# Optimization experiments

Hardware: AMD Instinct MI355X
Metric: run time of the kernel (lower is better)

Reference implementation:

```python
import jax, jax.numpy as jnp
import numpy as np

# ---- model / data constants ----
B, N, D, L = 32, 96, 64, 5          # graphs, nodes per graph, hidden, layers
EP = 768                             # directed edges per graph (symmetrized in to_dense)
NODE_VOCAB = 11                      # matches LocalFWL2(..., 11, 5, 'instance')
EDGE_VOCAB = 5                       # edge labels 0..4; index 5 = 'no edge' embedding row
EPS = 1e-5


def setup_inputs() -> dict:
    key = jax.random.key(0)
    ks = jax.random.split(key, 12)
    # block-contiguous batch: graph b owns nodes [b*N, (b+1)*N)
    x = jax.random.randint(ks[0], (B * N,), 0, NODE_VOCAB)
    u = jax.random.randint(ks[1], (B, EP), 0, N)
    v = jax.random.randint(ks[2], (B, EP), 0, N)
    off = (jnp.arange(B) * N)[:, None]
    edge_index = jnp.stack([(u + off).reshape(-1), (v + off).reshape(-1)], axis=0)
    edge_attr = jax.random.randint(ks[3], (B * EP,), 0, EDGE_VOCAB)
    s = 0.1
    inv = 1.0 / np.sqrt(D)
    return {
        "x": x,
        "edge_index": edge_index,
        "edge_attr": edge_attr,
        "node_emb": jax.random.normal(ks[4], (NODE_VOCAB, D), jnp.float32) * s,
        "edge_emb": jax.random.normal(ks[5], (EDGE_VOCAB + 1, D), jnp.float32) * s,
        "W1": jax.random.normal(ks[6], (L, D, D), jnp.float32) * inv,
        "b1": jnp.zeros((L, D), jnp.float32),
        "W2": jax.random.normal(ks[7], (L, D, D), jnp.float32) * inv,
        "b2": jnp.zeros((L, D), jnp.float32),
        "Wm": jax.random.normal(ks[8], (L, D, D), jnp.float32) * inv,
        "bm": jnp.zeros((L, D), jnp.float32),
        "gamma": jnp.ones((L, D), jnp.float32),
        "beta": jnp.zeros((L, D), jnp.float32),
        "pool_w": jax.random.normal(ks[9], (D, 1), jnp.float32) * inv,
        "pool_b": jnp.zeros((1,), jnp.float32),
    }


def reference(x, edge_index, edge_attr, node_emb, edge_emb,
              W1, b1, W2, b2, Wm, bm, gamma, beta, pool_w, pool_b):
    # ---- to_dense: sparse edge list -> dense per-graph edge-label matrix ----
    g = edge_index[0] // N
    u = edge_index[0] % N
    v = edge_index[1] % N
    A = jnp.full((B, N, N), EDGE_VOCAB, dtype=jnp.int32)        # EDGE_VOCAB = no-edge
    ea = edge_attr.astype(jnp.int32)
    A = A.at[g, u, v].set(ea)
    A = A.at[g, v, u].set(ea)                                    # undirected
    adj = (A != EDGE_VOCAB).astype(node_emb.dtype)               # [B,N,N]

    # ---- pair-state init: W_uv = h_u + h_v + edge_emb(A_uv) ----
    H = node_emb[x.reshape(B, N)]                                # [B,N,D]
    W = H[:, :, None, :] + H[:, None, :, :] + edge_emb[A]        # [B,N,N,D]

    # ---- local FWL(2) layers ----
    for l in range(L):
        h1 = jax.nn.relu(jnp.einsum('buwd,de->buwe', W, W1[l]) + b1[l])
        h2 = jax.nn.relu(jnp.einsum('bwvd,de->bwve', W, W2[l]) + b2[l])
        # aggregate over w restricted to neighbors of v (local FWL2)
        M = jnp.einsum('buwd,bwv,bwvd->buvd', h1, adj, h2)       # [B,N,N,D]
        W = W + jnp.einsum('buvd,de->buve', M, Wm[l]) + bm[l]
        # instance norm over the pair dims (u,v), per graph, per channel
        mu = W.mean(axis=(1, 2), keepdims=True)
        var = W.var(axis=(1, 2), keepdims=True)
        W = gamma[l] * (W - mu) * jax.lax.rsqrt(var + EPS) + beta[l]
        W = jax.nn.relu(W)

    # ---- pooling: sum over all pairs, then Linear(D, 1), squeeze ----
    pooled = W.sum(axis=(1, 2))                                  # [B,D]
    return (pooled @ pool_w + pool_b).squeeze(-1)                # [B]
```

## Files before the change

### kernel.cpp

```cpp
#include <hip/hip_runtime.h>
#include <hip/hip_bf16.h>

#define B_ 32
#define N_ 96
#define D_ 64
#define L_ 5
#define BE_ 24576
#define NN_ 9216
#define BNN_ 294912
#define EPS_ 1e-5f
#define INV_NN (1.0f/9216.0f)

typedef unsigned short u16;
typedef unsigned int u32;
typedef __attribute__((ext_vector_type(8))) short bf16x8;
typedef __attribute__((ext_vector_type(4))) float f32x4;

__device__ __forceinline__ float bf2f(u16 r){ return __uint_as_float(((u32)r) << 16); }
__device__ __forceinline__ u32 f2bf(float f){
  u32 u = __float_as_uint(f);
  return (u + 0x7fffu + ((u >> 16) & 1u)) >> 16;
}
__device__ __forceinline__ u32 pack2(float lo, float hi){
  return f2bf(lo) | (f2bf(hi) << 16);
}

__global__ void k_scatter(const int* __restrict__ ei, const int* __restrict__ ea,
                          int* __restrict__ A)
{
  int e = blockIdx.x * 256 + threadIdx.x;
  if (e >= BE_) return;
  int a = ei[e], bnode = ei[BE_ + e];
  int g = a / N_;
  int u = a % N_;
  int v = bnode % N_;
  int lab = ea[e] & 7;
  int base = g * NN_;
  atomicMax(&A[base + u * N_ + v], ((e + 1) << 3) | lab);
  atomicMax(&A[base + v * N_ + u], ((BE_ + e + 1) << 3) | lab);
}

__launch_bounds__(256)
__global__ void k_winit(const int* __restrict__ x, const int* __restrict__ A,
                        const float* __restrict__ nemb, const float* __restrict__ eemb,
                        u16* __restrict__ W)
{
  int gid = blockIdx.x * 256 + threadIdx.x;
  int d = (gid & 31) * 2;
  int p = gid >> 5;
  int b = p / NN_;
  int rem = p % NN_;
  int u = rem / N_;
  int v = rem % N_;
  int xu = x[b * N_ + u], xv = x[b * N_ + v];
  int pk = A[p];
  int lab = pk ? (pk & 7) : 5;
  float v0 = nemb[xu * 64 + d]     + nemb[xv * 64 + d]     + eemb[lab * 64 + d];
  float v1 = nemb[xu * 64 + d + 1] + nemb[xv * 64 + d + 1] + eemb[lab * 64 + d + 1];
  ((u32*)W)[gid] = pack2(v0, v1);
}

__global__ void k_prep(const float* __restrict__ W1, const float* __restrict__ W2,
                       const float* __restrict__ Wm, u16* __restrict__ WT)
{
  int idx = blockIdx.x * 256 + threadIdx.x;
  if (idx >= 15 * 4096) return;
  int l3 = idx >> 12;
  int r  = idx & 4095;
  int e = r >> 6, d = r & 63;
  int l = l3 / 3, which = l3 % 3;
  const float* s = which == 0 ? W1 : which == 1 ? W2 : Wm;
  WT[idx] = (u16)f2bf(s[l * 4096 + d * 64 + e]);
}

__global__ void k_ns(const float* __restrict__ st, const float* __restrict__ gm,
                     const float* __restrict__ bt, float* __restrict__ ns)
{
  int i = blockIdx.x * 256 + threadIdx.x;
  if (i >= B_ * 64) return;
  int d = i & 63;
  float S1 = st[i * 2], S2 = st[i * 2 + 1];
  float mu = S1 * INV_NN;
  float var = fmaf(S2, INV_NN, -mu * mu);
  float rsig = rsqrtf(var + EPS_);
  float sc = gm[d] * rsig;
  ns[i * 2] = sc;
  ns[i * 2 + 1] = fmaf(-mu, sc, bt[d]);
}

__launch_bounds__(256)
__global__ void k_lin2(const u16* __restrict__ W, const u16* __restrict__ WT1,
                       const u16* __restrict__ WT2,
                       const float* __restrict__ b1l, const float* __restrict__ b2l,
                       const int* __restrict__ A, const float* __restrict__ ns,
                       int use_norm, u16* __restrict__ h1, u16* __restrict__ g2)
{
  __shared__ u16 Cs[64 * 264];
  const int tid = threadIdx.x;
  const int wave = tid >> 6, lane = tid & 63;
  const int lm = lane & 15, lg = lane >> 4;
  const int b = blockIdx.x / 36;
  const int qbase = (blockIdx.x % 36) * 256;

  float sc[2][8], sh[2][8];
  if (use_norm) {
    #pragma unroll
    for (int s = 0; s < 2; ++s)
      #pragma unroll
      for (int jj = 0; jj < 8; jj += 2) {
        float4 t = *(const float4*)(ns + ((size_t)b * 64 + s * 32 + lg * 8 + jj) * 2);
        sc[s][jj] = t.x; sh[s][jj] = t.y; sc[s][jj + 1] = t.z; sh[s][jj + 1] = t.w;
      }
  } else {
    #pragma unroll
    for (int s = 0; s < 2; ++s)
      #pragma unroll
      for (int j = 0; j < 8; ++j) { sc[s][j] = 1.f; sh[s][j] = 0.f; }
  }

  bf16x8 bF[4][2];
  int flags[4];
  #pragma unroll
  for (int qt = 0; qt < 4; ++qt) {
    int q = qbase + wave * 64 + qt * 16 + lm;
    const u16* wrow = W + ((size_t)b * NN_ + q) * 64;
    flags[qt] = A[b * NN_ + q];
    #pragma unroll
    for (int s = 0; s < 2; ++s) {
      bf16x8 raw = *(const bf16x8*)(wrow + s * 32 + lg * 8);
      if (use_norm) {
        bf16x8 bb;
        #pragma unroll
        for (int j = 0; j < 8; ++j) {
          float v = bf2f((u16)raw[j]);
          v = fmaxf(fmaf(v, sc[s][j], sh[s][j]), 0.f);
          bb[j] = (short)f2bf(v);
        }
        bF[qt][s] = bb;
      } else {
        bF[qt][s] = raw;
      }
    }
  }

  const f32x4 zf = {0.f, 0.f, 0.f, 0.f};

  {
    bf16x8 aF[4][2];
    #pragma unroll
    for (int et = 0; et < 4; ++et)
      #pragma unroll
      for (int s = 0; s < 2; ++s)
        aF[et][s] = *(const bf16x8*)(WT1 + (et * 16 + lm) * 64 + s * 32 + lg * 8);
    f32x4 acc[4][4];
    #pragma unroll
    for (int i = 0; i < 4; ++i)
      #pragma unroll
      for (int j = 0; j < 4; ++j) acc[i][j] = zf;
    #pragma unroll
    for (int qt = 0; qt < 4; ++qt)
      #pragma unroll
      for (int s = 0; s < 2; ++s)
        #pragma unroll
        for (int et = 0; et < 4; ++et)
          acc[qt][et] = __builtin_amdgcn_mfma_f32_16x16x32_bf16(aF[et][s], bF[qt][s], acc[qt][et], 0, 0, 0);
    #pragma unroll
    for (int et = 0; et < 4; ++et) {
      float4 bs = *(const float4*)(b1l + et * 16 + lg * 4);
      float bv[4] = {bs.x, bs.y, bs.z, bs.w};
      #pragma unroll
      for (int qt = 0; qt < 4; ++qt) {
        int col = wave * 64 + qt * 16 + lm;
        #pragma unroll
        for (int r = 0; r < 4; ++r)
          Cs[(et * 16 + lg * 4 + r) * 264 + col] = (u16)f2bf(fmaxf(acc[qt][et][r] + bv[r], 0.f));
      }
    }
  }
  __syncthreads();
  {
    u16* ob = h1 + (size_t)b * 64 * NN_ + qbase;
    for (int i = tid; i < 2048; i += 256) {
      int e = i >> 5, qc = (i & 31) * 8;
      uint4 val = *(const uint4*)&Cs[e * 264 + qc];
      *(uint4*)(ob + (size_t)e * NN_ + qc) = val;
    }
  }
  __syncthreads();

  {
    bf16x8 aF[4][2];
    #pragma unroll
    for (int et = 0; et < 4; ++et)
      #pragma unroll
      for (int s = 0; s < 2; ++s)
        aF[et][s] = *(const bf16x8*)(WT2 + (et * 16 + lm) * 64 + s * 32 + lg * 8);
    f32x4 acc[4][4];
    #pragma unroll
    for (int i = 0; i < 4; ++i)
      #pragma unroll
      for (int j = 0; j < 4; ++j) acc[i][j] = zf;
    #pragma unroll
    for (int qt = 0; qt < 4; ++qt)
      #pragma unroll
      for (int s = 0; s < 2; ++s)
        #pragma unroll
        for (int et = 0; et < 4; ++et)
          acc[qt][et] = __builtin_amdgcn_mfma_f32_16x16x32_bf16(aF[et][s], bF[qt][s], acc[qt][et], 0, 0, 0);
    #pragma unroll
    for (int et = 0; et < 4; ++et) {
      float4 bs = *(const float4*)(b2l + et * 16 + lg * 4);
      float bv[4] = {bs.x, bs.y, bs.z, bs.w};
      #pragma unroll
      for (int qt = 0; qt < 4; ++qt) {
        int col = wave * 64 + qt * 16 + lm;
        #pragma unroll
        for (int r = 0; r < 4; ++r) {
          float v = fmaxf(acc[qt][et][r] + bv[r], 0.f);
          if (!flags[qt]) v = 0.f;
          Cs[(et * 16 + lg * 4 + r) * 264 + col] = (u16)f2bf(v);
        }
      }
    }
  }
  __syncthreads();
  {
    u16* ob = g2 + (size_t)b * 64 * NN_ + qbase;
    for (int i = tid; i < 2048; i += 256) {
      int e = i >> 5, qc = (i & 31) * 8;
      uint4 val = *(const uint4*)&Cs[e * 264 + qc];
      *(uint4*)(ob + (size_t)e * NN_ + qc) = val;
    }
  }
}

__launch_bounds__(256)
__global__ void k_einsum(const u16* __restrict__ h1, const u16* __restrict__ g2n,
                         u16* __restrict__ M)
{
  __shared__ u32 Bt[96 * 60];
  u16* Cst = (u16*)Bt;
  const int tid = threadIdx.x;
  const int wave = tid >> 6, lane = tid & 63;
  const int lm = lane & 15, lg = lane >> 4;
  const int bd = blockIdx.x;
  const u16* h1p = h1 + (size_t)bd * NN_;
  const u16* g2p = g2n + (size_t)bd * NN_;
  const int u0 = (wave & 1) * 48, v0 = (wave >> 1) * 48;

  #pragma unroll
  for (int it = 0; it < 9; ++it) {
    int p = it * 256 + tid;
    int wp = p / 48, vh = (p % 48) * 2;
    u32 a = *(const u32*)(g2p + (2 * wp) * 96 + vh);
    u32 c = *(const u32*)(g2p + (2 * wp + 1) * 96 + vh);
    Bt[vh * 60 + wp]       = (a & 0xffffu) | (c << 16);
    Bt[(vh + 1) * 60 + wp] = (a >> 16) | (c & 0xffff0000u);
  }
  __syncthreads();

  bf16x8 aF[3][3];
  #pragma unroll
  for (int t = 0; t < 3; ++t)
    #pragma unroll
    for (int s = 0; s < 3; ++s)
      aF[t][s] = *(const bf16x8*)(h1p + (u0 + t * 16 + lm) * 96 + s * 32 + lg * 8);

  bf16x8 bF[3][3];
  #pragma unroll
  for (int vt = 0; vt < 3; ++vt)
    #pragma unroll
    for (int s = 0; s < 3; ++s)
      bF[vt][s] = *(const bf16x8*)&Bt[(v0 + vt * 16 + lm) * 60 + s * 16 + lg * 4];
  __syncthreads();

  const f32x4 zf = {0.f, 0.f, 0.f, 0.f};
  f32x4 acc[3][3];
  #pragma unroll
  for (int i = 0; i < 3; ++i)
    #pragma unroll
    for (int j = 0; j < 3; ++j) acc[i][j] = zf;
  #pragma unroll
  for (int s = 0; s < 3; ++s)
    #pragma unroll
    for (int ut = 0; ut < 3; ++ut)
      #pragma unroll
      for (int vt = 0; vt < 3; ++vt)
        acc[ut][vt] = __builtin_amdgcn_mfma_f32_16x16x32_bf16(aF[ut][s], bF[vt][s], acc[ut][vt], 0, 0, 0);

  #pragma unroll
  for (int ut = 0; ut < 3; ++ut)
    #pragma unroll
    for (int vt = 0; vt < 3; ++vt)
      #pragma unroll
      for (int r = 0; r < 4; ++r)
        Cst[(u0 + ut * 16 + lg * 4 + r) * 104 + v0 + vt * 16 + lm] = (u16)f2bf(acc[ut][vt][r]);
  __syncthreads();
  u16* Mp = M + (size_t)bd * NN_;
  for (int i = tid; i < 1152; i += 256) {
    int u = i / 12, vc = (i % 12) * 8;
    uint4 val = *(const uint4*)&Cst[u * 104 + vc];
    *(uint4*)(Mp + u * 96 + vc) = val;
  }
}

__launch_bounds__(256)
__global__ void k_update(const u16* __restrict__ M, const u16* __restrict__ WmT,
                         const float* __restrict__ bml, u16* __restrict__ W,
                         const float* __restrict__ ns, int use_norm,
                         float* __restrict__ sto)
{
  __shared__ u16 Mt[128 * 64];
  __shared__ float red[128];
  const int tid = threadIdx.x;
  const int wave = tid >> 6, lane = tid & 63;
  const int lm = lane & 15, lg = lane >> 4;
  const int b = blockIdx.x / 72;
  const int qblk = (blockIdx.x % 72) * 128;

  if (tid < 128) red[tid] = 0.f;

  {
    const int ql = (tid & 63) + ((tid >> 6) & 1) * 64;
    const int d0 = (tid >> 7) * 32;
    const size_t gbase = (size_t)(b * 64) * NN_ + qblk + ql;
    #pragma unroll
    for (int dd = 0; dd < 32; ++dd) {
      int d = d0 + dd;
      u16 m = M[gbase + (size_t)d * NN_];
      int swz = (d >> 3) ^ (ql & 7);
      Mt[ql * 64 + swz * 8 + (d & 7)] = m;
    }
  }
  __syncthreads();

  bf16x8 aF[4][2];
  #pragma unroll
  for (int et = 0; et < 4; ++et)
    #pragma unroll
    for (int s = 0; s < 2; ++s)
      aF[et][s] = *(const bf16x8*)(WmT + (et * 16 + lm) * 64 + s * 32 + lg * 8);

  const f32x4 zf = {0.f, 0.f, 0.f, 0.f};
  f32x4 acc[2][4];
  #pragma unroll
  for (int i = 0; i < 2; ++i)
    #pragma unroll
    for (int j = 0; j < 4; ++j) acc[i][j] = zf;

  #pragma unroll
  for (int qtL = 0; qtL < 2; ++qtL) {
    int ql = (wave * 2 + qtL) * 16 + lm;
    bf16x8 bF[2];
    #pragma unroll
    for (int s = 0; s < 2; ++s) {
      int slot = s * 4 + lg;
      bF[s] = *(const bf16x8*)&Mt[ql * 64 + ((slot ^ (ql & 7)) * 8)];
    }
    #pragma unroll
    for (int s = 0; s < 2; ++s)
      #pragma unroll
      for (int et = 0; et < 4; ++et)
        acc[qtL][et] = __builtin_amdgcn_mfma_f32_16x16x32_bf16(aF[et][s], bF[s], acc[qtL][et], 0, 0, 0);
  }

  float s1[4][4], s2[4][4];
  #pragma unroll
  for (int i = 0; i < 4; ++i)
    #pragma unroll
    for (int j = 0; j < 4; ++j) { s1[i][j] = 0.f; s2[i][j] = 0.f; }

  #pragma unroll
  for (int et = 0; et < 4; ++et) {
    float4 bs = *(const float4*)(bml + et * 16 + lg * 4);
    float bv[4] = {bs.x, bs.y, bs.z, bs.w};
    float scn[4], shn[4];
    if (use_norm) {
      float4 t0 = *(const float4*)(ns + ((size_t)b * 64 + et * 16 + lg * 4) * 2);
      float4 t1 = *(const float4*)(ns + ((size_t)b * 64 + et * 16 + lg * 4) * 2 + 4);
      scn[0] = t0.x; shn[0] = t0.y; scn[1] = t0.z; shn[1] = t0.w;
      scn[2] = t1.x; shn[2] = t1.y; scn[3] = t1.z; shn[3] = t1.w;
    } else {
      #pragma unroll
      for (int r = 0; r < 4; ++r) { scn[r] = 1.f; shn[r] = 0.f; }
    }
    #pragma unroll
    for (int qtL = 0; qtL < 2; ++qtL) {
      int qg = qblk + (wave * 2 + qtL) * 16 + lm;
      u16* Wp = W + ((size_t)b * NN_ + qg) * 64 + et * 16 + lg * 4;
      uint2 wo = *(const uint2*)Wp;
      float wv[4] = {bf2f((u16)(wo.x & 0xffff)), bf2f((u16)(wo.x >> 16)),
                     bf2f((u16)(wo.y & 0xffff)), bf2f((u16)(wo.y >> 16))};
      float o[4];
      #pragma unroll
      for (int r = 0; r < 4; ++r) {
        float res = use_norm ? fmaxf(fmaf(wv[r], scn[r], shn[r]), 0.f) : wv[r];
        float val = acc[qtL][et][r] + bv[r] + res;
        o[r] = val;
        s1[et][r] += val;
        s2[et][r] = fmaf(val, val, s2[et][r]);
      }
      uint2 ov;
      ov.x = pack2(o[0], o[1]);
      ov.y = pack2(o[2], o[3]);
      *(uint2*)Wp = ov;
    }
  }

  #pragma unroll
  for (int et = 0; et < 4; ++et)
    #pragma unroll
    for (int r = 0; r < 4; ++r) {
      float a = s1[et][r], c = s2[et][r];
      a += __shfl_xor(a, 1, 64); a += __shfl_xor(a, 2, 64);
      a += __shfl_xor(a, 4, 64); a += __shfl_xor(a, 8, 64);
      c += __shfl_xor(c, 1, 64); c += __shfl_xor(c, 2, 64);
      c += __shfl_xor(c, 4, 64); c += __shfl_xor(c, 8, 64);
      if (lm == 0) {
        int e = et * 16 + lg * 4 + r;
        atomicAdd(&red[e], a);
        atomicAdd(&red[64 + e], c);
      }
    }
  __syncthreads();
  if (tid < 64) atomicAdd(&sto[((size_t)b * 64 + tid) * 2], red[tid]);
  else if (tid < 128) atomicAdd(&sto[((size_t)b * 64 + (tid - 64)) * 2 + 1], red[tid]);
}

__launch_bounds__(256)
__global__ void k_pool(const u16* __restrict__ W,
                       const float* __restrict__ st,
                       const float* __restrict__ gml, const float* __restrict__ btl,
                       const float* __restrict__ pw, const float* __restrict__ pb,
                       float* __restrict__ out)
{
  const int b = blockIdx.x / 24;
  const int chunk = blockIdx.x % 24;
  const int tid = threadIdx.x;
  const int e = tid & 63;
  float S1 = st[(b * 64 + e) * 2], S2 = st[(b * 64 + e) * 2 + 1];
  float mu = S1 * INV_NN;
  float var = fmaf(S2, INV_NN, -mu * mu);
  float rsig = rsqrtf(var + EPS_);
  float scl = gml[e] * rsig;
  float shf = fmaf(-mu, scl, btl[e]);
  float pwv = pw[e];
  const u16* base = W + (size_t)b * NN_ * 64 + chunk * 24576;
  float s = 0.f;
  for (int k = 0; k < 96; k++) {
    float w = bf2f(base[k * 256 + tid]);
    s += fmaxf(fmaf(w, scl, shf), 0.f) * pwv;
  }
  for (int o = 32; o; o >>= 1) s += __shfl_down(s, o, 64);
  __shared__ float rs[4];
  if ((tid & 63) == 0) rs[tid >> 6] = s;
  __syncthreads();
  if (tid == 0) {
    float t = rs[0] + rs[1] + rs[2] + rs[3];
    if (chunk == 0) t += pb[0];
    atomicAdd(&out[b], t);
  }
}

extern "C" void kernel_launch(void* const* d_in, const int* in_sizes, int n_in,
                              void* d_out, int out_size, void* d_ws, size_t ws_size,
                              hipStream_t stream) {
  const int*   x    = (const int*)d_in[0];
  const int*   ei   = (const int*)d_in[1];
  const int*   ea   = (const int*)d_in[2];
  const float* nemb = (const float*)d_in[3];
  const float* eemb = (const float*)d_in[4];
  const float* W1   = (const float*)d_in[5];
  const float* b1   = (const float*)d_in[6];
  const float* W2   = (const float*)d_in[7];
  const float* b2   = (const float*)d_in[8];
  const float* Wm   = (const float*)d_in[9];
  const float* bm   = (const float*)d_in[10];
  const float* gm   = (const float*)d_in[11];
  const float* bt   = (const float*)d_in[12];
  const float* pw   = (const float*)d_in[13];
  const float* pb   = (const float*)d_in[14];

  char* ws = (char*)d_ws;
  const size_t OFF_A  = 0;
  const size_t OFF_W  = 1179648;
  const size_t OFF_H1 = 38928384;
  const size_t OFF_G2 = 76677120;
  const size_t OFF_M  = 114425856;
  const size_t OFF_ST = 152174592;
  const size_t OFF_NS = 152190976;
  const size_t OFF_WT = 152207360;
  const size_t NEED   = OFF_WT + 122880;
  if (ws_size < NEED) return;

  int*   A     = (int*)(ws + OFF_A);
  u16*   W     = (u16*)(ws + OFF_W);
  u16*   h1    = (u16*)(ws + OFF_H1);
  u16*   g2n   = (u16*)(ws + OFF_G2);
  u16*   M     = (u16*)(ws + OFF_M);
  float* stats = (float*)(ws + OFF_ST);
  float* ns    = (float*)(ws + OFF_NS);
  u16*   WT    = (u16*)(ws + OFF_WT);
  float* out   = (float*)d_out;

  hipMemsetAsync(A, 0, 1179648, stream);
  hipMemsetAsync(stats, 0, 16384, stream);
  hipMemsetAsync(out, 0, 32 * sizeof(float), stream);

  k_prep<<<240, 256, 0, stream>>>(W1, W2, Wm, WT);
  k_scatter<<<96, 256, 0, stream>>>(ei, ea, A);
  k_winit<<<36864, 256, 0, stream>>>(x, A, nemb, eemb, W);

  for (int l = 0; l < L_; l++) {
    int un = (l > 0);
    if (un) {
      k_ns<<<8, 256, 0, stream>>>(stats, gm + (l - 1) * 64, bt + (l - 1) * 64, ns);
      hipMemsetAsync(stats, 0, 16384, stream);
    }
    k_lin2<<<1152, 256, 0, stream>>>(W, WT + (l * 3 + 0) * 4096, WT + (l * 3 + 1) * 4096,
                                     b1 + l * 64, b2 + l * 64, A, ns, un, h1, g2n);
    k_einsum<<<2048, 256, 0, stream>>>(h1, g2n, M);
    k_update<<<2304, 256, 0, stream>>>(M, WT + (l * 3 + 2) * 4096, bm + l * 64, W, ns, un, stats);
  }
  k_pool<<<768, 256, 0, stream>>>(W, stats, gm + 4 * 64, bt + 4 * 64, pw, pb, out);
}
```

Before: 624.0 us.

## Fold norm-stat kernel into consumers, per-layer stats buffers, vectorize M transpose load

Removes the separate k_ns kernel and the per-layer stats memset by computing scale/shift inline in k_lin2 and k_update from per-layer stats slices. This cuts launch and serialization overhead between layers. k_update now loads M with 16-byte vector reads and uses a new two-level XOR swizzle when scattering into shared memory, replacing 32 scalar strided u16 loads per thread. In k_einsum one barrier is moved after the global h1 fragment loads so they overlap the transpose. The cost is some redundant rsqrt math in every block.

```diff
diff --git a/kernel.cpp b/kernel.cpp
--- a/kernel.cpp
+++ b/kernel.cpp
@@ -73,26 +73,13 @@
   WT[idx] = (u16)f2bf(s[l * 4096 + d * 64 + e]);
 }
 
-__global__ void k_ns(const float* __restrict__ st, const float* __restrict__ gm,
-                     const float* __restrict__ bt, float* __restrict__ ns)
-{
-  int i = blockIdx.x * 256 + threadIdx.x;
-  if (i >= B_ * 64) return;
-  int d = i & 63;
-  float S1 = st[i * 2], S2 = st[i * 2 + 1];
-  float mu = S1 * INV_NN;
-  float var = fmaf(S2, INV_NN, -mu * mu);
-  float rsig = rsqrtf(var + EPS_);
-  float sc = gm[d] * rsig;
-  ns[i * 2] = sc;
-  ns[i * 2 + 1] = fmaf(-mu, sc, bt[d]);
-}
-
 __launch_bounds__(256)
 __global__ void k_lin2(const u16* __restrict__ W, const u16* __restrict__ WT1,
                        const u16* __restrict__ WT2,
                        const float* __restrict__ b1l, const float* __restrict__ b2l,
-                       const int* __restrict__ A, const float* __restrict__ ns,
+                       const int* __restrict__ A,
+                       const float* __restrict__ stp, const float* __restrict__ gml,
+                       const float* __restrict__ btl,
                        int use_norm, u16* __restrict__ h1, u16* __restrict__ g2)
 {
   __shared__ u16 Cs[64 * 264];
@@ -105,12 +92,25 @@
   float sc[2][8], sh[2][8];
   if (use_norm) {
     #pragma unroll
-    for (int s = 0; s < 2; ++s)
-      #pragma unroll
-      for (int jj = 0; jj < 8; jj += 2) {
-        float4 t = *(const float4*)(ns + ((size_t)b * 64 + s * 32 + lg * 8 + jj) * 2);
-        sc[s][jj] = t.x; sh[s][jj] = t.y; sc[s][jj + 1] = t.z; sh[s][jj + 1] = t.w;
-      }
+    for (int s = 0; s < 2; ++s) {
+      int d0 = s * 32 + lg * 8;
+      #pragma unroll
+      for (int j = 0; j < 8; j += 2) {
+        float4 t = *(const float4*)(stp + ((size_t)b * 64 + d0 + j) * 2);
+        float2 g = *(const float2*)(gml + d0 + j);
+        float2 bb = *(const float2*)(btl + d0 + j);
+        float mu0 = t.x * INV_NN;
+        float var0 = fmaf(t.y, INV_NN, -mu0 * mu0);
+        float s0 = g.x * rsqrtf(var0 + EPS_);
+        sc[s][j] = s0;
+        sh[s][j] = fmaf(-mu0, s0, bb.x);
+        float mu1 = t.z * INV_NN;
+        float var1 = fmaf(t.w, INV_NN, -mu1 * mu1);
+        float s1v = g.y * rsqrtf(var1 + EPS_);
+        sc[s][j + 1] = s1v;
+        sh[s][j + 1] = fmaf(-mu1, s1v, bb.y);
+      }
+    }
   } else {
     #pragma unroll
     for (int s = 0; s < 2; ++s)
@@ -257,7 +257,6 @@
     Bt[vh * 60 + wp]       = (a & 0xffffu) | (c << 16);
     Bt[(vh + 1) * 60 + wp] = (a >> 16) | (c & 0xffff0000u);
   }
-  __syncthreads();
 
   bf16x8 aF[3][3];
   #pragma unroll
@@ -265,6 +264,7 @@
     #pragma unroll
     for (int s = 0; s < 3; ++s)
       aF[t][s] = *(const bf16x8*)(h1p + (u0 + t * 16 + lm) * 96 + s * 32 + lg * 8);
+  __syncthreads();
 
   bf16x8 bF[3][3];
   #pragma unroll
@@ -307,7 +307,8 @@
 __launch_bounds__(256)
 __global__ void k_update(const u16* __restrict__ M, const u16* __restrict__ WmT,
                          const float* __restrict__ bml, u16* __restrict__ W,
-                         const float* __restrict__ ns, int use_norm,
+                         const float* __restrict__ stp, const float* __restrict__ gml,
+                         const float* __restrict__ btl, int use_norm,
                          float* __restrict__ sto)
 {
   __shared__ u16 Mt[128 * 64];
@@ -320,26 +321,34 @@
 
   if (tid < 128) red[tid] = 0.f;
 
-  {
-    const int ql = (tid & 63) + ((tid >> 6) & 1) * 64;
-    const int d0 = (tid >> 7) * 32;
-    const size_t gbase = (size_t)(b * 64) * NN_ + qblk + ql;
-    #pragma unroll
-    for (int dd = 0; dd < 32; ++dd) {
-      int d = d0 + dd;
-      u16 m = M[gbase + (size_t)d * NN_];
-      int swz = (d >> 3) ^ (ql & 7);
-      Mt[ql * 64 + swz * 8 + (d & 7)] = m;
-    }
-  }
-  __syncthreads();
-
   bf16x8 aF[4][2];
   #pragma unroll
   for (int et = 0; et < 4; ++et)
     #pragma unroll
     for (int s = 0; s < 2; ++s)
       aF[et][s] = *(const bf16x8*)(WmT + (et * 16 + lm) * 64 + s * 32 + lg * 8);
+
+  {
+    const int dpl = tid >> 2;
+    const int qob = tid & 3;
+    const u16* Mb = M + (size_t)(b * 64 + dpl) * NN_ + qblk;
+    #pragma unroll
+    for (int t = 0; t < 4; ++t) {
+      int qo = qob + t * 4;
+      uint4 v = *(const uint4*)(Mb + qo * 8);
+      u32 ws[4] = {v.x, v.y, v.z, v.w};
+      #pragma unroll
+      for (int h = 0; h < 4; ++h) {
+        int j0 = h * 2;
+        int q0 = qo * 8 + j0;
+        int slot0 = (dpl >> 3) ^ j0 ^ (qo & 7);
+        int slot1 = (dpl >> 3) ^ (j0 + 1) ^ (qo & 7);
+        Mt[q0 * 64 + slot0 * 8 + (dpl & 7)]       = (u16)(ws[h] & 0xffffu);
+        Mt[(q0 + 1) * 64 + slot1 * 8 + (dpl & 7)] = (u16)(ws[h] >> 16);
+      }
+    }
+  }
+  __syncthreads();
 
   const f32x4 zf = {0.f, 0.f, 0.f, 0.f};
   f32x4 acc[2][4];
@@ -354,8 +363,8 @@
     bf16x8 bF[2];
     #pragma unroll
     for (int s = 0; s < 2; ++s) {
-      int slot = s * 4 + lg;
-      bF[s] = *(const bf16x8*)&Mt[ql * 64 + ((slot ^ (ql & 7)) * 8)];
+      int slot = (s * 4 + lg) ^ (ql & 7) ^ ((ql >> 3) & 7);
+      bF[s] = *(const bf16x8*)&Mt[ql * 64 + slot * 8];
     }
     #pragma unroll
     for (int s = 0; s < 2; ++s)
@@ -372,14 +381,27 @@
 
   #pragma unroll
   for (int et = 0; et < 4; ++et) {
-    float4 bs = *(const float4*)(bml + et * 16 + lg * 4);
+    int e0 = et * 16 + lg * 4;
+    float4 bs = *(const float4*)(bml + e0);
     float bv[4] = {bs.x, bs.y, bs.z, bs.w};
     float scn[4], shn[4];
     if (use_norm) {
-      float4 t0 = *(const float4*)(ns + ((size_t)b * 64 + et * 16 + lg * 4) * 2);
-      float4 t1 = *(const float4*)(ns + ((size_t)b * 64 + et * 16 + lg * 4) * 2 + 4);
-      scn[0] = t0.x; shn[0] = t0.y; scn[1] = t0.z; shn[1] = t0.w;
-      scn[2] = t1.x; shn[2] = t1.y; scn[3] = t1.z; shn[3] = t1.w;
+      float4 t0 = *(const float4*)(stp + ((size_t)b * 64 + e0) * 2);
+      float4 t1 = *(const float4*)(stp + ((size_t)b * 64 + e0) * 2 + 4);
+      float4 gv = *(const float4*)(gml + e0);
+      float4 bv2 = *(const float4*)(btl + e0);
+      float S1v[4] = {t0.x, t0.z, t1.x, t1.z};
+      float S2v[4] = {t0.y, t0.w, t1.y, t1.w};
+      float gvv[4] = {gv.x, gv.y, gv.z, gv.w};
+      float btv[4] = {bv2.x, bv2.y, bv2.z, bv2.w};
+      #pragma unroll
+      for (int r = 0; r < 4; ++r) {
+        float mu = S1v[r] * INV_NN;
+        float var = fmaf(S2v[r], INV_NN, -mu * mu);
+        float s0 = gvv[r] * rsqrtf(var + EPS_);
+        scn[r] = s0;
+        shn[r] = fmaf(-mu, s0, btv[r]);
+      }
     } else {
       #pragma unroll
       for (int r = 0; r < 4; ++r) { scn[r] = 1.f; shn[r] = 0.f; }
@@ -387,7 +409,7 @@
     #pragma unroll
     for (int qtL = 0; qtL < 2; ++qtL) {
       int qg = qblk + (wave * 2 + qtL) * 16 + lm;
-      u16* Wp = W + ((size_t)b * NN_ + qg) * 64 + et * 16 + lg * 4;
+      u16* Wp = W + ((size_t)b * NN_ + qg) * 64 + e0;
       uint2 wo = *(const uint2*)Wp;
       float wv[4] = {bf2f((u16)(wo.x & 0xffff)), bf2f((u16)(wo.x >> 16)),
                      bf2f((u16)(wo.y & 0xffff)), bf2f((u16)(wo.y >> 16))};
@@ -488,8 +510,7 @@
   const size_t OFF_G2 = 76677120;
   const size_t OFF_M  = 114425856;
   const size_t OFF_ST = 152174592;
-  const size_t OFF_NS = 152190976;
-  const size_t OFF_WT = 152207360;
+  const size_t OFF_WT = 152256512;
   const size_t NEED   = OFF_WT + 122880;
   if (ws_size < NEED) return;
 
@@ -499,12 +520,11 @@
   u16*   g2n   = (u16*)(ws + OFF_G2);
   u16*   M     = (u16*)(ws + OFF_M);
   float* stats = (float*)(ws + OFF_ST);
-  float* ns    = (float*)(ws + OFF_NS);
   u16*   WT    = (u16*)(ws + OFF_WT);
   float* out   = (float*)d_out;
 
   hipMemsetAsync(A, 0, 1179648, stream);
-  hipMemsetAsync(stats, 0, 16384, stream);
+  hipMemsetAsync(stats, 0, 81920, stream);
   hipMemsetAsync(out, 0, 32 * sizeof(float), stream);
 
   k_prep<<<240, 256, 0, stream>>>(W1, W2, Wm, WT);
@@ -513,14 +533,16 @@
 
   for (int l = 0; l < L_; l++) {
     int un = (l > 0);
-    if (un) {
-      k_ns<<<8, 256, 0, stream>>>(stats, gm + (l - 1) * 64, bt + (l - 1) * 64, ns);
-      hipMemsetAsync(stats, 0, 16384, stream);
-    }
+    const float* stp = un ? stats + (size_t)(l - 1) * 4096 : stats;
+    const float* gml = un ? gm + (l - 1) * 64 : gm;
+    const float* btl = un ? bt + (l - 1) * 64 : bt;
+    float* sto = stats + (size_t)l * 4096;
     k_lin2<<<1152, 256, 0, stream>>>(W, WT + (l * 3 + 0) * 4096, WT + (l * 3 + 1) * 4096,
-                                     b1 + l * 64, b2 + l * 64, A, ns, un, h1, g2n);
+                                     b1 + l * 64, b2 + l * 64, A, stp, gml, btl, un, h1, g2n);
     k_einsum<<<2048, 256, 0, stream>>>(h1, g2n, M);
-    k_update<<<2304, 256, 0, stream>>>(M, WT + (l * 3 + 2) * 4096, bm + l * 64, W, ns, un, stats);
-  }
-  k_pool<<<768, 256, 0, stream>>>(W, stats, gm + 4 * 64, bt + 4 * 64, pw, pb, out);
-}
+    k_update<<<2304, 256, 0, stream>>>(M, WT + (l * 3 + 2) * 4096, bm + l * 64, W,
+                                       stp, gml, btl, un, sto);
+  }
+  k_pool<<<768, 256, 0, stream>>>(W, stats + 4 * 4096, gm + 4 * 64, bt + 4 * 64,
+                                  pw, pb, out);
+}
```

Result: no change. 615.3 us (-1.4%).
